# Kernel optimization log

Measured on AMD Instinct MI355X. Metric: run time of the kernel, lower is better.

Reference implementation:

```python
import jax, jax.numpy as jnp
import numpy as np

N_HEAD = 16
ROPE_BASE = 10000.0


def _rope_cache(T, head_dim):
    # half-split RoPE: cos/sin of shape [T, head_dim//2]
    half = head_dim // 2
    inv_freq = ROPE_BASE ** (-jnp.arange(half, dtype=jnp.float32) / half)
    angles = jnp.arange(T, dtype=jnp.float32)[:, None] * inv_freq[None, :]  # [T, half]
    return jnp.cos(angles), jnp.sin(angles)


def _apply_rope(x, cos, sin):
    # x: [B, H, T, D]; cos/sin: [T, D//2]
    half = x.shape[-1] // 2
    x1, x2 = x[..., :half], x[..., half:]
    c = cos[None, None, :, :]
    s = sin[None, None, :, :]
    return jnp.concatenate([x1 * c - x2 * s, x1 * s + x2 * c], axis=-1)


def setup_inputs() -> dict:
    key = jax.random.key(0)
    k1, k2, k3 = jax.random.split(key, 3)
    B, T, C = 2, 2048, 1024
    x = jax.random.normal(k1, (B, T, C), dtype=jnp.float32)
    w_attn = jax.random.normal(k2, (C, 3 * C), dtype=jnp.float32) * (C ** -0.5)
    b_attn = jnp.zeros((3 * C,), dtype=jnp.float32)
    w_proj = jax.random.normal(k3, (C, C), dtype=jnp.float32) * (C ** -0.5)
    b_proj = jnp.zeros((C,), dtype=jnp.float32)
    return {"x": x, "w_attn": w_attn, "b_attn": b_attn, "w_proj": w_proj, "b_proj": b_proj}


def reference(x, w_attn, b_attn, w_proj, b_proj):
    B, T, C = x.shape
    H = N_HEAD
    hd = C // H

    qkv = x @ w_attn + b_attn                      # [B, T, 3C] fused QKV
    q, k, v = jnp.split(qkv, 3, axis=-1)
    q = q.reshape(B, T, H, hd).transpose(0, 2, 1, 3)  # [B, H, T, hd]
    k = k.reshape(B, T, H, hd).transpose(0, 2, 1, 3)
    v = v.reshape(B, T, H, hd).transpose(0, 2, 1, 3)

    cos, sin = _rope_cache(T, hd)
    q = _apply_rope(q, cos, sin)
    k = _apply_rope(k, cos, sin)

    scale = 1.0 / jnp.sqrt(jnp.float32(hd))
    att = jnp.einsum("bhqd,bhkd->bhqk", q, k) * scale  # [B, H, T, T]
    causal = jnp.tril(jnp.ones((T, T), dtype=bool))
    att = jnp.where(causal[None, None], att, -jnp.inf)
    att = jax.nn.softmax(att, axis=-1)
    y = jnp.einsum("bhqk,bhkd->bhqd", att, v)          # [B, H, T, hd]
    y = y.transpose(0, 2, 1, 3).reshape(B, T, C)
    return y @ w_proj + b_proj
```

## Files before the change

kernel.cpp:

```cpp
#include <hip/hip_runtime.h>
#include <hip/hip_bf16.h>
#include <cmath>

typedef _Float16 half_t;
typedef half_t half4 __attribute__((ext_vector_type(4)));
typedef half_t half8 __attribute__((ext_vector_type(8)));
typedef float f32x4 __attribute__((ext_vector_type(4)));

#define N_HEADS 16
#define HD      64
#define T_SEQ   2048
#define B_SZ    2
#define C_DIM   1024
#define M_ROWS  (B_SZ * T_SEQ)
#define N_QKV   (3 * C_DIM)
#define QSCALE  0.18033688f

__device__ inline void load_lds16(const half_t* g, half_t* l) {
  __builtin_amdgcn_global_load_lds(
      (const __attribute__((address_space(1))) void*)g,
      (__attribute__((address_space(3))) void*)l, 16, 0, 0);
}

__global__ __launch_bounds__(256) void k_prep(const float* __restrict__ x,
                                              half_t* __restrict__ xb,
                                              const float* __restrict__ wa,
                                              half_t* __restrict__ wT,
                                              const float* __restrict__ wp,
                                              half_t* __restrict__ wpT) {
  __shared__ float tile[64][65];
  int bid = blockIdx.x, tid = threadIdx.x;
  if (bid < 4096) {
    int i = (bid * 256 + tid) * 4;
    float4 v = *(const float4*)(x + i);
    half_t o[4] = {(half_t)v.x, (half_t)v.y, (half_t)v.z, (half_t)v.w};
    *(ulong1*)(xb + i) = *(ulong1*)o;
    return;
  }
  const float* in; half_t* out; int K, N, id;
  if (bid < 4096 + 768) { id = bid - 4096; in = wa; out = wT;  K = 1024; N = 3072; }
  else                  { id = bid - 4864; in = wp; out = wpT; K = 1024; N = 1024; }
  int n0 = (id % (N / 64)) * 64, k0 = (id / (N / 64)) * 64;
  int tx = tid & 63, ty = tid >> 6;
  #pragma unroll
  for (int i = 0; i < 64; i += 4)
    tile[ty + i][tx] = in[(size_t)(k0 + ty + i) * N + n0 + tx];
  __syncthreads();
  #pragma unroll
  for (int i = 0; i < 64; i += 4) {
    int r = ty + i;
    out[(size_t)(n0 + r) * K + k0 + tx] = (half_t)tile[tx][r];
  }
}

template <typename OT, int TN>
__global__ __launch_bounds__(256) void k_gemm(const half_t* __restrict__ A,
                                              const half_t* __restrict__ Bt,
                                              const float* __restrict__ bias,
                                              OT* __restrict__ C,
                                              int M, int N, int K) {
  constexpr int NI = TN / 32;
  __shared__ half_t As[128 * 64];
  __shared__ half_t Bs[TN * 64];
  int tid = threadIdx.x;
  int wave = tid >> 6, lane = tid & 63;
  int lane15 = lane & 15, quad = lane >> 4;
  int wm = (wave >> 1) * 64, wn = (wave & 1) * (TN / 2);
  int bm0 = blockIdx.y * 128, bn0 = blockIdx.x * TN;
  f32x4 acc[4][NI] = {};

  for (int kb = 0; kb < K; kb += 64) {
    const half_t* Ag = A + (size_t)bm0 * K + kb;
    const half_t* Bg = Bt + (size_t)bn0 * K + kb;
    __syncthreads();
    #pragma unroll
    for (int p = 0; p < 4; p++) {
      int fc = wave * 4 * 64 + p * 64 + lane;
      int r = fc >> 3, c = (fc & 7) ^ (r & 7);
      load_lds16(Ag + (size_t)r * K + c * 8, As + (wave * 4 + p) * 512);
    }
    #pragma unroll
    for (int p = 0; p < NI; p++) {
      int fc = wave * NI * 64 + p * 64 + lane;
      int r = fc >> 3, c = (fc & 7) ^ (r & 7);
      load_lds16(Bg + (size_t)r * K + c * 8, Bs + (wave * NI + p) * 512);
    }
    __syncthreads();
    #pragma unroll
    for (int ks = 0; ks < 2; ks++) {
      half8 af[4], bf[NI];
      #pragma unroll
      for (int i = 0; i < 4; i++) {
        int Ra = wm + i * 16 + lane15;
        af[i] = *(const half8*)(As + Ra * 64 + ((ks * 4 + quad) ^ (Ra & 7)) * 8);
      }
      #pragma unroll
      for (int i = 0; i < NI; i++) {
        int Rb = wn + i * 16 + lane15;
        bf[i] = *(const half8*)(Bs + Rb * 64 + ((ks * 4 + quad) ^ (Rb & 7)) * 8);
      }
      #pragma unroll
      for (int mi = 0; mi < 4; mi++)
        #pragma unroll
        for (int ni = 0; ni < NI; ni++)
          acc[mi][ni] = __builtin_amdgcn_mfma_f32_16x16x32_f16(af[mi], bf[ni], acc[mi][ni], 0, 0, 0);
    }
  }
  #pragma unroll
  for (int mi = 0; mi < 4; mi++)
    #pragma unroll
    for (int ni = 0; ni < NI; ni++) {
      int n = bn0 + wn + ni * 16 + lane15;
      float bv = bias[n];
      int mrow = bm0 + wm + mi * 16 + quad * 4;
      #pragma unroll
      for (int r = 0; r < 4; r++)
        C[(size_t)(mrow + r) * N + n] = (OT)(acc[mi][ni][r] + bv);
    }
}

__global__ __launch_bounds__(256) void k_rope(const half_t* __restrict__ qkv,
                                              half_t* __restrict__ Q,
                                              half_t* __restrict__ Ko,
                                              half_t* __restrict__ Vt) {
  __shared__ float vt[64][65];
  int bh = blockIdx.y;
  int b = bh >> 4, h = bh & 15;
  int t0 = blockIdx.x * 64;
  int tid = threadIdx.x;
  int trow = tid >> 5, i = tid & 31;
  float inv = exp2f(-(float)i * (13.287712379549449f / 32.0f));
  #pragma unroll
  for (int p = 0; p < 8; p++) {
    int tloc = p * 8 + trow;
    int t = t0 + tloc;
    const half_t* row = qkv + (size_t)(b * T_SEQ + t) * N_QKV;
    float q1 = (float)row[h * 64 + i],        q2 = (float)row[h * 64 + i + 32];
    float k1 = (float)row[1024 + h * 64 + i], k2 = (float)row[1024 + h * 64 + i + 32];
    float v1 = (float)row[2048 + h * 64 + i], v2 = (float)row[2048 + h * 64 + i + 32];
    float s, c;
    sincosf((float)t * inv, &s, &c);
    size_t base = ((size_t)bh * T_SEQ + t) * HD;
    Q[base + i]       = (half_t)((q1 * c - q2 * s) * QSCALE);
    Q[base + i + 32]  = (half_t)((q1 * s + q2 * c) * QSCALE);
    Ko[base + i]      = (half_t)(k1 * c - k2 * s);
    Ko[base + i + 32] = (half_t)(k1 * s + k2 * c);
    vt[i][tloc]      = v1;
    vt[i + 32][tloc] = v2;
  }
  __syncthreads();
  int d = tid >> 6, tc = tid & 63;
  #pragma unroll
  for (int p = 0; p < 16; p++) {
    int dd = p * 4 + d;
    Vt[((size_t)bh * HD + dd) * T_SEQ + t0 + tc] = (half_t)vt[dd][tc];
  }
}

__global__ __launch_bounds__(256) void k_flash(const half_t* __restrict__ Qg,
                                               const half_t* __restrict__ Kg,
                                               const half_t* __restrict__ Vg,
                                               half_t* __restrict__ y) {
  __shared__ float Ored[4][32][65];
  __shared__ float Lred[4][64];
  int bh = blockIdx.y;
  int b = bh >> 4, h = bh & 15;
  int tid = threadIdx.x;
  int wave = tid >> 6, lane = tid & 63;
  int lane15 = lane & 15, quad = lane >> 4;
  const half_t* Qb = Qg + (size_t)bh * T_SEQ * HD;
  const half_t* Kb = Kg + (size_t)bh * T_SEQ * HD;
  const half_t* Vb = Vg + (size_t)bh * HD * T_SEQ;
  const half4 ones = {(half_t)1.f, (half_t)1.f, (half_t)1.f, (half_t)1.f};
  const half_t* Kw = Kb + (size_t)(wave * 16 + lane15) * HD;
  int vcol = wave * 16 + quad * 4;

  #pragma unroll
  for (int phase = 0; phase < 2; phase++) {
    int qt = phase == 0 ? (int)blockIdx.x : (31 - (int)blockIdx.x);
    int q0 = qt * 64;
    half8 bq[4][2];
    #pragma unroll
    for (int qf = 0; qf < 4; qf++) {
      const half_t* qp = Qb + (size_t)(q0 + qf * 16 + lane15) * HD;
      bq[qf][0] = *(const half8*)(qp + quad * 8);
      bq[qf][1] = *(const half8*)(qp + 32 + quad * 8);
    }
    f32x4 ot[4][4] = {};
    f32x4 lacc[4] = {};

    half8 ak0 = *(const half8*)(Kw + quad * 8);
    half8 ak1 = *(const half8*)(Kw + 32 + quad * 8);
    half4 av[4];
    #pragma unroll
    for (int nm = 0; nm < 4; nm++)
      av[nm] = *(const half4*)(Vb + (size_t)(nm * 16 + lane15) * T_SEQ + vcol);

    for (int j = 0; j <= qt; j++) {
      int kv0 = j * 64;
      f32x4 sacc[4];
      #pragma unroll
      for (int qf = 0; qf < 4; qf++) {
        f32x4 z = {};
        z = __builtin_amdgcn_mfma_f32_16x16x32_f16(ak0, bq[qf][0], z, 0, 0, 0);
        sacc[qf] = __builtin_amdgcn_mfma_f32_16x16x32_f16(ak1, bq[qf][1], z, 0, 0, 0);
      }
      int kvn = (j < qt) ? kv0 + 64 : kv0;
      half8 an0 = *(const half8*)(Kw + (size_t)kvn * HD + quad * 8);
      half8 an1 = *(const half8*)(Kw + (size_t)kvn * HD + 32 + quad * 8);
      half4 avn[4];
      #pragma unroll
      for (int nm = 0; nm < 4; nm++)
        avn[nm] = *(const half4*)(Vb + (size_t)(nm * 16 + lane15) * T_SEQ + kvn + vcol);

      bool diag = (j == qt);
      half4 bp[4];
      #pragma unroll
      for (int qf = 0; qf < 4; qf++) {
        #pragma unroll
        for (int r = 0; r < 4; r++) {
          float sv = sacc[qf][r];
          if (diag && (wave * 16 + quad * 4 + r > qf * 16 + lane15)) sv = -1.0e30f;
          bp[qf][r] = (half_t)exp2f(fminf(sv, 14.0f));
        }
        lacc[qf] = __builtin_amdgcn_mfma_f32_16x16x16f16(ones, bp[qf], lacc[qf], 0, 0, 0);
      }
      #pragma unroll
      for (int nm = 0; nm < 4; nm++)
        #pragma unroll
        for (int qf = 0; qf < 4; qf++)
          ot[nm][qf] = __builtin_amdgcn_mfma_f32_16x16x16f16(av[nm], bp[qf], ot[nm][qf], 0, 0, 0);
      ak0 = an0; ak1 = an1;
      #pragma unroll
      for (int nm = 0; nm < 4; nm++) av[nm] = avn[nm];
    }

    int ql = tid >> 2, dg = (tid & 3) * 8;
    float invl = 0.f;
    #pragma unroll
    for (int hf = 0; hf < 2; hf++) {
      #pragma unroll
      for (int nm2 = 0; nm2 < 2; nm2++) {
        int nm = hf * 2 + nm2;
        #pragma unroll
        for (int qf = 0; qf < 4; qf++)
          #pragma unroll
          for (int r = 0; r < 4; r++)
            Ored[wave][nm2 * 16 + quad * 4 + r][qf * 16 + lane15] = ot[nm][qf][r];
      }
      if (hf == 0) {
        #pragma unroll
        for (int qf = 0; qf < 4; qf++)
          Lred[wave][qf * 16 + lane15] = lacc[qf][0];
      }
      __syncthreads();
      if (hf == 0)
        invl = 1.0f / (Lred[0][ql] + Lred[1][ql] + Lred[2][ql] + Lred[3][ql]);
      half8 o8;
      #pragma unroll
      for (int dd = 0; dd < 8; dd++) {
        float s = Ored[0][dg + dd][ql] + Ored[1][dg + dd][ql] +
                  Ored[2][dg + dd][ql] + Ored[3][dg + dd][ql];
        o8[dd] = (half_t)(s * invl);
      }
      *(half8*)(y + (size_t)(b * T_SEQ + q0 + ql) * C_DIM + h * 64 + hf * 32 + dg) = o8;
      __syncthreads();
    }
  }
}

extern "C" void kernel_launch(void* const* d_in, const int* in_sizes, int n_in,
                              void* d_out, int out_size, void* d_ws, size_t ws_size,
                              hipStream_t stream) {
  const float* x      = (const float*)d_in[0];
  const float* w_attn = (const float*)d_in[1];
  const float* b_attn = (const float*)d_in[2];
  const float* w_proj = (const float*)d_in[3];
  const float* b_proj = (const float*)d_in[4];
  float* out = (float*)d_out;

  char* ws = (char*)d_ws;
  const size_t MB = 1u << 20;
  half_t* xb  = (half_t*)(ws);
  half_t* wT  = (half_t*)(ws + 8 * MB);
  half_t* wpT = (half_t*)(ws + 14 * MB);
  half_t* Q   = (half_t*)(ws + 16 * MB);
  half_t* Kb  = (half_t*)(ws + 24 * MB);
  half_t* Vt  = (half_t*)(ws + 32 * MB);
  half_t* qkv = (half_t*)(ws + 40 * MB);
  half_t* y   = (half_t*)(ws + 40 * MB);

  k_prep<<<4096 + 768 + 256, 256, 0, stream>>>(x, xb, w_attn, wT, w_proj, wpT);
  k_gemm<half_t, 128><<<dim3(N_QKV / 128, M_ROWS / 128), 256, 0, stream>>>(
      xb, wT, b_attn, qkv, M_ROWS, N_QKV, C_DIM);
  k_rope<<<dim3(T_SEQ / 64, B_SZ * N_HEADS), 256, 0, stream>>>(qkv, Q, Kb, Vt);
  k_flash<<<dim3(16, B_SZ * N_HEADS), 256, 0, stream>>>(Q, Kb, Vt, y);
  k_gemm<float, 64><<<dim3(C_DIM / 64, M_ROWS / 128), 256, 0, stream>>>(
      y, wpT, b_proj, out, M_ROWS, C_DIM, C_DIM);
}
```

Before: 204.5 us.

## Stage K/V tiles in LDS with double-buffered async global_load_lds

The flash attention kernel now copies each 64-row K and V tile into a double-buffered, XOR-swizzled LDS region using global_load_lds. Each wave then reads its MFMA operands from LDS instead of issuing scattered per-lane global loads. The diagonal tile is peeled out of the loop so the causal mask test runs only there. The staging buffers share a union with the output reduction scratch, which adds a __syncthreads per KV step and depends on the async LDS loads having completed by that barrier.

```diff
diff --git a/kernel.cpp b/kernel.cpp
--- a/kernel.cpp
+++ b/kernel.cpp
@@ -161,8 +161,10 @@
                                                const half_t* __restrict__ Kg,
                                                const half_t* __restrict__ Vg,
                                                half_t* __restrict__ y) {
-  __shared__ float Ored[4][32][65];
-  __shared__ float Lred[4][64];
+  __shared__ union {
+    struct { half_t K[2][4096]; half_t V[2][4096]; } s;
+    struct { float O[4][32][65]; float L[4][64]; } r;
+  } u;
   int bh = blockIdx.y;
   int b = bh >> 4, h = bh & 15;
   int tid = threadIdx.x;
@@ -172,8 +174,30 @@
   const half_t* Kb = Kg + (size_t)bh * T_SEQ * HD;
   const half_t* Vb = Vg + (size_t)bh * HD * T_SEQ;
   const half4 ones = {(half_t)1.f, (half_t)1.f, (half_t)1.f, (half_t)1.f};
-  const half_t* Kw = Kb + (size_t)(wave * 16 + lane15) * HD;
-  int vcol = wave * 16 + quad * 4;
+
+  int Rk = wave * 16 + lane15;
+  int kOff0 = (Rk * 8 + ((quad) ^ (Rk & 7))) * 8;
+  int kOff1 = (Rk * 8 + ((4 + quad) ^ (Rk & 7))) * 8;
+  int vcc = wave * 2 + (quad >> 1);
+  int vOff[4];
+  #pragma unroll
+  for (int nm = 0; nm < 4; nm++) {
+    int Rv = nm * 16 + lane15;
+    vOff[nm] = (Rv * 8 + (vcc ^ (Rv & 7))) * 8 + (quad & 1) * 4;
+  }
+
+  #define STAGE(buf, kv0)                                                      \
+    {                                                                          \
+      _Pragma("unroll")                                                        \
+      for (int pp = 0; pp < 2; pp++) {                                         \
+        int fc = (wave * 2 + pp) * 64 + lane;                                  \
+        int rr = fc >> 3, cc = (fc & 7) ^ (rr & 7);                            \
+        load_lds16(Kb + (size_t)((kv0) + rr) * HD + cc * 8,                    \
+                   &u.s.K[buf][0] + fc * 8);                                   \
+        load_lds16(Vb + (size_t)rr * T_SEQ + (kv0) + cc * 8,                   \
+                   &u.s.V[buf][0] + fc * 8);                                   \
+      }                                                                        \
+    }
 
   #pragma unroll
   for (int phase = 0; phase < 2; phase++) {
@@ -189,15 +213,15 @@
     f32x4 ot[4][4] = {};
     f32x4 lacc[4] = {};
 
-    half8 ak0 = *(const half8*)(Kw + quad * 8);
-    half8 ak1 = *(const half8*)(Kw + 32 + quad * 8);
-    half4 av[4];
-    #pragma unroll
-    for (int nm = 0; nm < 4; nm++)
-      av[nm] = *(const half4*)(Vb + (size_t)(nm * 16 + lane15) * T_SEQ + vcol);
-
-    for (int j = 0; j <= qt; j++) {
-      int kv0 = j * 64;
+    STAGE(0, 0);
+    for (int j = 0; j < qt; j++) {
+      int buf = j & 1;
+      __syncthreads();
+      STAGE(buf ^ 1, (j + 1) * 64);
+      const half_t* Kt = &u.s.K[buf][0];
+      const half_t* Vt = &u.s.V[buf][0];
+      half8 ak0 = *(const half8*)(Kt + kOff0);
+      half8 ak1 = *(const half8*)(Kt + kOff1);
       f32x4 sacc[4];
       #pragma unroll
       for (int qf = 0; qf < 4; qf++) {
@@ -205,35 +229,57 @@
         z = __builtin_amdgcn_mfma_f32_16x16x32_f16(ak0, bq[qf][0], z, 0, 0, 0);
         sacc[qf] = __builtin_amdgcn_mfma_f32_16x16x32_f16(ak1, bq[qf][1], z, 0, 0, 0);
       }
-      int kvn = (j < qt) ? kv0 + 64 : kv0;
-      half8 an0 = *(const half8*)(Kw + (size_t)kvn * HD + quad * 8);
-      half8 an1 = *(const half8*)(Kw + (size_t)kvn * HD + 32 + quad * 8);
-      half4 avn[4];
-      #pragma unroll
-      for (int nm = 0; nm < 4; nm++)
-        avn[nm] = *(const half4*)(Vb + (size_t)(nm * 16 + lane15) * T_SEQ + kvn + vcol);
-
-      bool diag = (j == qt);
+      half4 bp[4];
+      #pragma unroll
+      for (int qf = 0; qf < 4; qf++) {
+        #pragma unroll
+        for (int r = 0; r < 4; r++)
+          bp[qf][r] = (half_t)exp2f(fminf(sacc[qf][r], 14.0f));
+        lacc[qf] = __builtin_amdgcn_mfma_f32_16x16x16f16(ones, bp[qf], lacc[qf], 0, 0, 0);
+      }
+      #pragma unroll
+      for (int nm = 0; nm < 4; nm++) {
+        half4 av = *(const half4*)(Vt + vOff[nm]);
+        #pragma unroll
+        for (int qf = 0; qf < 4; qf++)
+          ot[nm][qf] = __builtin_amdgcn_mfma_f32_16x16x16f16(av, bp[qf], ot[nm][qf], 0, 0, 0);
+      }
+    }
+
+    {
+      int buf = qt & 1;
+      __syncthreads();
+      const half_t* Kt = &u.s.K[buf][0];
+      const half_t* Vt = &u.s.V[buf][0];
+      half8 ak0 = *(const half8*)(Kt + kOff0);
+      half8 ak1 = *(const half8*)(Kt + kOff1);
+      f32x4 sacc[4];
+      #pragma unroll
+      for (int qf = 0; qf < 4; qf++) {
+        f32x4 z = {};
+        z = __builtin_amdgcn_mfma_f32_16x16x32_f16(ak0, bq[qf][0], z, 0, 0, 0);
+        sacc[qf] = __builtin_amdgcn_mfma_f32_16x16x32_f16(ak1, bq[qf][1], z, 0, 0, 0);
+      }
       half4 bp[4];
       #pragma unroll
       for (int qf = 0; qf < 4; qf++) {
         #pragma unroll
         for (int r = 0; r < 4; r++) {
           float sv = sacc[qf][r];
-          if (diag && (wave * 16 + quad * 4 + r > qf * 16 + lane15)) sv = -1.0e30f;
+          if (wave * 16 + quad * 4 + r > qf * 16 + lane15) sv = -1.0e30f;
           bp[qf][r] = (half_t)exp2f(fminf(sv, 14.0f));
         }
         lacc[qf] = __builtin_amdgcn_mfma_f32_16x16x16f16(ones, bp[qf], lacc[qf], 0, 0, 0);
       }
       #pragma unroll
-      for (int nm = 0; nm < 4; nm++)
+      for (int nm = 0; nm < 4; nm++) {
+        half4 av = *(const half4*)(Vt + vOff[nm]);
         #pragma unroll
         for (int qf = 0; qf < 4; qf++)
-          ot[nm][qf] = __builtin_amdgcn_mfma_f32_16x16x16f16(av[nm], bp[qf], ot[nm][qf], 0, 0, 0);
-      ak0 = an0; ak1 = an1;
-      #pragma unroll
-      for (int nm = 0; nm < 4; nm++) av[nm] = avn[nm];
-    }
+          ot[nm][qf] = __builtin_amdgcn_mfma_f32_16x16x16f16(av, bp[qf], ot[nm][qf], 0, 0, 0);
+      }
+    }
+    __syncthreads();
 
     int ql = tid >> 2, dg = (tid & 3) * 8;
     float invl = 0.f;
@@ -246,27 +292,28 @@
         for (int qf = 0; qf < 4; qf++)
           #pragma unroll
           for (int r = 0; r < 4; r++)
-            Ored[wave][nm2 * 16 + quad * 4 + r][qf * 16 + lane15] = ot[nm][qf][r];
+            u.r.O[wave][nm2 * 16 + quad * 4 + r][qf * 16 + lane15] = ot[nm][qf][r];
       }
       if (hf == 0) {
         #pragma unroll
         for (int qf = 0; qf < 4; qf++)
-          Lred[wave][qf * 16 + lane15] = lacc[qf][0];
+          u.r.L[wave][qf * 16 + lane15] = lacc[qf][0];
       }
       __syncthreads();
       if (hf == 0)
-        invl = 1.0f / (Lred[0][ql] + Lred[1][ql] + Lred[2][ql] + Lred[3][ql]);
+        invl = 1.0f / (u.r.L[0][ql] + u.r.L[1][ql] + u.r.L[2][ql] + u.r.L[3][ql]);
       half8 o8;
       #pragma unroll
       for (int dd = 0; dd < 8; dd++) {
-        float s = Ored[0][dg + dd][ql] + Ored[1][dg + dd][ql] +
-                  Ored[2][dg + dd][ql] + Ored[3][dg + dd][ql];
+        float s = u.r.O[0][dg + dd][ql] + u.r.O[1][dg + dd][ql] +
+                  u.r.O[2][dg + dd][ql] + u.r.O[3][dg + dd][ql];
         o8[dd] = (half_t)(s * invl);
       }
       *(half8*)(y + (size_t)(b * T_SEQ + q0 + ql) * C_DIM + h * 64 + hf * 32 + dg) = o8;
       __syncthreads();
     }
   }
+  #undef STAGE
 }
 
 extern "C" void kernel_launch(void* const* d_in, const int* in_sizes, int n_in,
```

After: 204.5 us. Within noise of the previous version (+0.0%).
